# Optimization experiments

Hardware: AMD Instinct MI355X
Metric: run time of the kernel (lower is better)

## Reference

```python
import jax, jax.numpy as jnp
import numpy as np
import math

B, S, D = 4, 2048, 1024
H = 1
HD = D // H  # head_dim == hidden_dim since num_heads=1 (required by source's phase_encoder Linear)
HALF = HD // 2
SYNC_LOSS_WEIGHT = 0.01


def setup_inputs() -> dict:
    key = jax.random.key(0)
    ks = jax.random.split(key, 11)
    wstd = 0.02
    inp = {
        "x": jax.random.normal(ks[0], (B, S, D), dtype=jnp.float32),
        "Wq": jax.random.normal(ks[1], (D, D), dtype=jnp.float32) * wstd,
        "bq": jnp.zeros((D,), jnp.float32),
        "Wk": jax.random.normal(ks[2], (D, D), dtype=jnp.float32) * wstd,
        "bk": jnp.zeros((D,), jnp.float32),
        "Wv": jax.random.normal(ks[3], (D, D), dtype=jnp.float32) * wstd,
        "bv": jnp.zeros((D,), jnp.float32),
        "Wp": jax.random.normal(ks[4], (D, D), dtype=jnp.float32) * wstd,
        "bp": jnp.zeros((D,), jnp.float32),
        "Wo": jax.random.normal(ks[5], (D, D), dtype=jnp.float32) * wstd,
        "bo": jnp.zeros((D,), jnp.float32),
        "bifurcation_param": jnp.asarray(1.0, jnp.float32),
        "phase_coupling": jnp.asarray(0.5, jnp.float32),
    }
    return inp


def _phase(t, Wp, bp):
    # t: [B,H,S,HD] -> instantaneous phase via angle(complex(first_half, second_half))
    pf = t @ Wp.T + bp
    re, im = pf[..., :HALF], pf[..., HALF:]
    return jnp.arctan2(im, re)  # [B,H,S,HALF]


def reference(x, Wq, bq, Wk, bk, Wv, bv, Wp, bp, Wo, bo, bifurcation_param, phase_coupling):
    b, s, d = x.shape
    Q = (x @ Wq.T + bq).reshape(b, s, H, HD).transpose(0, 2, 1, 3)  # [B,H,S,HD]
    K = (x @ Wk.T + bk).reshape(b, s, H, HD).transpose(0, 2, 1, 3)
    V = (x @ Wv.T + bv).reshape(b, s, H, HD).transpose(0, 2, 1, 3)

    scores = jnp.einsum("bhqd,bhkd->bhqk", Q, K) / math.sqrt(HD)

    pQ = _phase(Q, Wp, bp)
    pK = _phase(K, Wp, bp)
    # mean_d cos(pQ - pK) == (cos(pQ)@cos(pK)^T + sin(pQ)@sin(pK)^T) / HALF
    sync = (jnp.einsum("bhqd,bhkd->bhqk", jnp.cos(pQ), jnp.cos(pK))
            + jnp.einsum("bhqd,bhkd->bhqk", jnp.sin(pQ), jnp.sin(pK))) / HALF

    t = jnp.tanh(scores)
    bif = bifurcation_param * t * (1.0 - t)

    chaotic = scores + phase_coupling * sync + bif
    attn = jax.nn.softmax(chaotic, axis=-1)

    av = jnp.einsum("bhqk,bhkd->bhqd", attn, V)
    av = av.transpose(0, 2, 1, 3).reshape(b, s, d)
    out = av @ Wo.T + bo

    # torch.var default: unbiased (ddof=1), over last dim of sync
    sync_loss = SYNC_LOSS_WEIGHT * jnp.var(sync, axis=-1, ddof=1).mean()
    return out, sync_loss
```

## Files before the change

### kernel.cpp

```cpp
#include <hip/hip_runtime.h>
#include <hip/hip_bf16.h>
#include <math.h>

#define S_LEN 2048
#define D_MODEL 1024
#define N_BATCH 4
#define N_HALF 512

typedef unsigned short u16;
typedef __attribute__((ext_vector_type(8))) short bf16x8;
typedef __attribute__((ext_vector_type(4))) float f32x4;

__device__ inline u16 f2bf(float v) {
  __hip_bfloat16 h = __float2bfloat16(v);
  return *reinterpret_cast<u16*>(&h);
}
__device__ inline float bf2f(u16 u) {
  __hip_bfloat16 h = *reinterpret_cast<__hip_bfloat16*>(&u);
  return __bfloat162float(h);
}
__device__ inline void gl2lds16(const void* g, void* l) {
  __builtin_amdgcn_global_load_lds(
      (const __attribute__((address_space(1))) unsigned int*)g,
      (__attribute__((address_space(3))) unsigned int*)l, 16, 0, 0);
}
__device__ inline float fast_tanh(float x) {
  float e = __expf(2.0f * x);
  return 1.0f - 2.0f / (e + 1.0f);
}

__global__ __launch_bounds__(256)
void cast_bf4(const float* __restrict__ src, u16* __restrict__ dst, long long n4) {
  long long i = (long long)blockIdx.x * 256 + threadIdx.x;
  if (i >= n4) return;
  float4 v = ((const float4*)src)[i];
  ushort4 o;
  o.x = f2bf(v.x); o.y = f2bf(v.y); o.z = f2bf(v.z); o.w = f2bf(v.w);
  ((ushort4*)dst)[i] = o;
}
__global__ __launch_bounds__(256)
void cast_split(const float* __restrict__ src, u16* __restrict__ hi,
                u16* __restrict__ lo, long long n) {
  long long i = (long long)blockIdx.x * 256 + threadIdx.x;
  if (i < n) {
    float v = src[i];
    u16 h = f2bf(v);
    hi[i] = h;
    lo[i] = f2bf(v - bf2f(h));
  }
}
__global__ __launch_bounds__(256)
void transpose_split(const float* __restrict__ src, u16* __restrict__ hi,
                     u16* __restrict__ lo) {
  __shared__ float t[32][33];
  const int bx = blockIdx.x * 32;
  const int by = blockIdx.y * 32;
  const int c = threadIdx.x & 31;
  const int r0 = (threadIdx.x >> 5) * 4;
#pragma unroll
  for (int r = 0; r < 4; r++)
    t[r0 + r][c] = src[(long long)(by + r0 + r) * D_MODEL + bx + c];
  __syncthreads();
#pragma unroll
  for (int r = 0; r < 4; r++) {
    float v = t[c][r0 + r];
    long long idx = (long long)(bx + r0 + r) * D_MODEL + by + c;
    u16 h = f2bf(v);
    hi[idx] = h;
    lo[idx] = f2bf(v - bf2f(h));
  }
}
__global__ __launch_bounds__(256)
void zero_stats(float* __restrict__ p, int n) {
  int i = blockIdx.x * 256 + threadIdx.x;
  if (i < n) p[i] = 0.f;
}
__global__ __launch_bounds__(256)
void w2_bias(const float* __restrict__ Wo, const float* __restrict__ bv,
             float* __restrict__ w2b) {
  const int d = blockIdx.x;
  const int tid = threadIdx.x;
  float acc = 0.f;
  for (int j = tid; j < D_MODEL; j += 256)
    acc += Wo[(long long)d * D_MODEL + j] * bv[j];
#pragma unroll
  for (int m = 1; m < 64; m <<= 1) acc += __shfl_xor(acc, m);
  __shared__ float red[4];
  if ((tid & 63) == 0) red[tid >> 6] = acc;
  __syncthreads();
  if (tid == 0) w2b[d] = red[0] + red[1] + red[2] + red[3];
}

__global__ __launch_bounds__(256, 2)
void qk_fused(const u16* __restrict__ X, const u16* __restrict__ Wq,
              const u16* __restrict__ Wk,
              const float* __restrict__ bq, const float* __restrict__ bk,
              u16* __restrict__ Qo, u16* __restrict__ Ko) {
  __shared__ u16 Xs[128 * 32];
  __shared__ u16 Qs[128 * 32];
  __shared__ u16 Ks[128 * 32];
  const int tid  = threadIdx.x;
  const int wave = tid >> 6;
  const int lane = tid & 63;
  const int quad = lane >> 4;
  const int tc   = lane & 15;
  const int bm = blockIdx.y * 128;
  const int bn = blockIdx.x * 128;
  const int wm = (wave & 1) * 64;
  const int wn = (wave >> 1) * 64;

  f32x4 acc1[4][4], acc2[4][4];
#pragma unroll
  for (int i = 0; i < 4; i++)
#pragma unroll
    for (int j = 0; j < 4; j++) {
      acc1[i][j] = (f32x4){0.f, 0.f, 0.f, 0.f};
      acc2[i][j] = (f32x4){0.f, 0.f, 0.f, 0.f};
    }

  const int srow = wave * 32 + (lane >> 2);
  const int scol = (lane & 3) * 8;
  const u16* gx = X  + (long long)(bm + srow) * D_MODEL + scol;
  const u16* gq = Wq + (long long)(bn + srow) * D_MODEL + scol;
  const u16* gk = Wk + (long long)(bn + srow) * D_MODEL + scol;
  const int wb = (wave * 32) * 32;
  const long long r16 = 16LL * D_MODEL;

  for (int k0 = 0; k0 < D_MODEL; k0 += 32) {
    gl2lds16(gx,       Xs + wb);
    gl2lds16(gx + r16, Xs + wb + 512);
    gl2lds16(gq,       Qs + wb);
    gl2lds16(gq + r16, Qs + wb + 512);
    gl2lds16(gk,       Ks + wb);
    gl2lds16(gk + r16, Ks + wb + 512);
    gx += 32; gq += 32; gk += 32;
    __syncthreads();
    bf16x8 af[4], bq4[4], bk4[4];
#pragma unroll
    for (int i = 0; i < 4; i++)
      af[i] = *(const bf16x8*)(Xs + (wm + i * 16 + tc) * 32 + quad * 8);
#pragma unroll
    for (int j = 0; j < 4; j++) {
      int o = (wn + j * 16 + tc) * 32 + quad * 8;
      bq4[j] = *(const bf16x8*)(Qs + o);
      bk4[j] = *(const bf16x8*)(Ks + o);
    }
#pragma unroll
    for (int i = 0; i < 4; i++)
#pragma unroll
      for (int j = 0; j < 4; j++) {
        acc1[i][j] = __builtin_amdgcn_mfma_f32_16x16x32_bf16(af[i], bq4[j], acc1[i][j], 0, 0, 0);
        acc2[i][j] = __builtin_amdgcn_mfma_f32_16x16x32_bf16(af[i], bk4[j], acc2[i][j], 0, 0, 0);
      }
    __syncthreads();
  }

#pragma unroll
  for (int i = 0; i < 4; i++) {
    const int row0 = bm + wm + i * 16 + quad * 4;
#pragma unroll
    for (int j = 0; j < 4; j++) {
      const int col = bn + wn + j * 16 + tc;
#pragma unroll
      for (int r = 0; r < 4; r++) {
        long long idx = (long long)(row0 + r) * D_MODEL + col;
        Qo[idx] = f2bf(acc1[i][j][r] + bq[col]);
        Ko[idx] = f2bf(acc2[i][j][r] + bk[col]);
      }
    }
  }
}

__global__ __launch_bounds__(256, 2)
void pf_fused(const u16* __restrict__ Qb, const u16* __restrict__ Wp,
              const float* __restrict__ bp,
              u16* __restrict__ pfQ, u16* __restrict__ pfK,
              long long TDo) {
  __shared__ u16 Qs[128 * 32];
  __shared__ u16 Ks[128 * 32];
  __shared__ u16 Ws[128 * 32];
  const int tid  = threadIdx.x;
  const int wave = tid >> 6;
  const int lane = tid & 63;
  const int quad = lane >> 4;
  const int tc   = lane & 15;
  const int bm = blockIdx.y * 128;
  const int bn = blockIdx.x * 128;
  const int wm = (wave & 1) * 64;
  const int wn = (wave >> 1) * 64;

  f32x4 acc1[4][4], acc2[4][4];
#pragma unroll
  for (int i = 0; i < 4; i++)
#pragma unroll
    for (int j = 0; j < 4; j++) {
      acc1[i][j] = (f32x4){0.f, 0.f, 0.f, 0.f};
      acc2[i][j] = (f32x4){0.f, 0.f, 0.f, 0.f};
    }

  const int srow = wave * 32 + (lane >> 2);
  const int scol = (lane & 3) * 8;
  const u16* gq = Qb + (long long)(bm + srow) * D_MODEL + scol;
  const u16* gk = gq + TDo;
  const u16* gw = Wp + (long long)(bn + srow) * D_MODEL + scol;
  const int wb = (wave * 32) * 32;
  const long long r16 = 16LL * D_MODEL;

  for (int k0 = 0; k0 < D_MODEL; k0 += 32) {
    gl2lds16(gq,       Qs + wb);
    gl2lds16(gq + r16, Qs + wb + 512);
    gl2lds16(gk,       Ks + wb);
    gl2lds16(gk + r16, Ks + wb + 512);
    gl2lds16(gw,       Ws + wb);
    gl2lds16(gw + r16, Ws + wb + 512);
    gq += 32; gk += 32; gw += 32;
    __syncthreads();
    bf16x8 aq[4], ak[4], bw[4];
#pragma unroll
    for (int i = 0; i < 4; i++) {
      int o = (wm + i * 16 + tc) * 32 + quad * 8;
      aq[i] = *(const bf16x8*)(Qs + o);
      ak[i] = *(const bf16x8*)(Ks + o);
    }
#pragma unroll
    for (int j = 0; j < 4; j++)
      bw[j] = *(const bf16x8*)(Ws + (wn + j * 16 + tc) * 32 + quad * 8);
#pragma unroll
    for (int i = 0; i < 4; i++)
#pragma unroll
      for (int j = 0; j < 4; j++) {
        acc1[i][j] = __builtin_amdgcn_mfma_f32_16x16x32_bf16(aq[i], bw[j], acc1[i][j], 0, 0, 0);
        acc2[i][j] = __builtin_amdgcn_mfma_f32_16x16x32_bf16(ak[i], bw[j], acc2[i][j], 0, 0, 0);
      }
    __syncthreads();
  }

#pragma unroll
  for (int i = 0; i < 4; i++) {
    const int row0 = bm + wm + i * 16 + quad * 4;
#pragma unroll
    for (int j = 0; j < 4; j++) {
      const int col = bn + wn + j * 16 + tc;
#pragma unroll
      for (int r = 0; r < 4; r++) {
        long long idx = (long long)(row0 + r) * D_MODEL + col;
        float b = bp[col];
        pfQ[idx] = f2bf(acc1[i][j][r] + b);
        pfK[idx] = f2bf(acc2[i][j][r] + b);
      }
    }
  }
}

__global__ __launch_bounds__(256)
void mfma_gemm_out3(const u16* __restrict__ Ah, const u16* __restrict__ Al,
                    const u16* __restrict__ Bh, const u16* __restrict__ Bl,
                    const float* __restrict__ bias, float* __restrict__ C,
                    int N, int K) {
  __shared__ u16 Ash[128 * 32];
  __shared__ u16 Asl[128 * 32];
  __shared__ u16 Bsh[128 * 32];
  __shared__ u16 Bsl[128 * 32];
  const int tid  = threadIdx.x;
  const int wave = tid >> 6;
  const int lane = tid & 63;
  const int quad = lane >> 4;
  const int tc   = lane & 15;
  const int bm = blockIdx.y * 128;
  const int bn = blockIdx.x * 128;
  const int wm = (wave & 1) * 64;
  const int wn = (wave >> 1) * 64;

  f32x4 acc[4][4];
#pragma unroll
  for (int i = 0; i < 4; i++)
#pragma unroll
    for (int j = 0; j < 4; j++) acc[i][j] = (f32x4){0.f, 0.f, 0.f, 0.f};

  const int srow = wave * 32 + (lane >> 2);
  const int scol = (lane & 3) * 8;
  long long aoff = (long long)(bm + srow) * K + scol;
  long long boff = (long long)(bn + srow) * K + scol;
  const u16 *gah = Ah + aoff, *gal = Al + aoff;
  const u16 *gbh = Bh + boff, *gbl = Bl + boff;
  const int wbase = (wave * 32) * 32;
  const long long r16K = 16LL * K;

  for (int k0 = 0; k0 < K; k0 += 32) {
    gl2lds16(gah,        Ash + wbase);
    gl2lds16(gah + r16K, Ash + wbase + 512);
    gl2lds16(gal,        Asl + wbase);
    gl2lds16(gal + r16K, Asl + wbase + 512);
    gl2lds16(gbh,        Bsh + wbase);
    gl2lds16(gbh + r16K, Bsh + wbase + 512);
    gl2lds16(gbl,        Bsl + wbase);
    gl2lds16(gbl + r16K, Bsl + wbase + 512);
    gah += 32; gal += 32; gbh += 32; gbl += 32;
    __syncthreads();
    bf16x8 ah[4], al[4], bh[4], bl[4];
#pragma unroll
    for (int i = 0; i < 4; i++) {
      int o = (wm + i * 16 + tc) * 32 + quad * 8;
      ah[i] = *(const bf16x8*)(Ash + o);
      al[i] = *(const bf16x8*)(Asl + o);
    }
#pragma unroll
    for (int j = 0; j < 4; j++) {
      int o = (wn + j * 16 + tc) * 32 + quad * 8;
      bh[j] = *(const bf16x8*)(Bsh + o);
      bl[j] = *(const bf16x8*)(Bsl + o);
    }
#pragma unroll
    for (int i = 0; i < 4; i++)
#pragma unroll
      for (int j = 0; j < 4; j++) {
        acc[i][j] = __builtin_amdgcn_mfma_f32_16x16x32_bf16(ah[i], bh[j], acc[i][j], 0, 0, 0);
        acc[i][j] = __builtin_amdgcn_mfma_f32_16x16x32_bf16(ah[i], bl[j], acc[i][j], 0, 0, 0);
        acc[i][j] = __builtin_amdgcn_mfma_f32_16x16x32_bf16(al[i], bh[j], acc[i][j], 0, 0, 0);
      }
    __syncthreads();
  }
#pragma unroll
  for (int i = 0; i < 4; i++) {
    const int row0 = bm + wm + i * 16 + quad * 4;
#pragma unroll
    for (int j = 0; j < 4; j++) {
      const int col = bn + wn + j * 16 + tc;
      float b = bias ? bias[col] : 0.f;
#pragma unroll
      for (int r = 0; r < 4; r++)
        C[(long long)(row0 + r) * N + col] = acc[i][j][r] + b;
    }
  }
}

__global__ __launch_bounds__(256)
void vwt_kernel(const u16* __restrict__ W2h, const u16* __restrict__ W2l,
                const u16* __restrict__ X, const float* __restrict__ w2b,
                u16* __restrict__ Ch, u16* __restrict__ Cl,
                long long sB, long long sC) {
  __shared__ u16 Ah[128 * 32];
  __shared__ u16 Al[128 * 32];
  __shared__ u16 Bs[128 * 32];
  const int tid  = threadIdx.x;
  const int wave = tid >> 6;
  const int lane = tid & 63;
  const int quad = lane >> 4;
  const int tc   = lane & 15;
  const int bm = blockIdx.y * 128;
  const int bn = blockIdx.x * 128;
  const long long z = blockIdx.z;
  const int wm = (wave & 1) * 64;
  const int wn = (wave >> 1) * 64;

  f32x4 acc[4][4];
#pragma unroll
  for (int i = 0; i < 4; i++)
#pragma unroll
    for (int j = 0; j < 4; j++) acc[i][j] = (f32x4){0.f, 0.f, 0.f, 0.f};

  const int srow = wave * 32 + (lane >> 2);
  const int scol = (lane & 3) * 8;
  const long long aoff = (long long)(bm + srow) * D_MODEL + scol;
  const u16* gah = W2h + aoff;
  const u16* gal = W2l + aoff;
  const u16* gb  = X + z * sB + (long long)(bn + srow) * D_MODEL + scol;
  const int wb = (wave * 32) * 32;
  const long long r16 = 16LL * D_MODEL;

  for (int k0 = 0; k0 < D_MODEL; k0 += 32) {
    gl2lds16(gah,       Ah + wb);
    gl2lds16(gah + r16, Ah + wb + 512);
    gl2lds16(gal,       Al + wb);
    gl2lds16(gal + r16, Al + wb + 512);
    gl2lds16(gb,        Bs + wb);
    gl2lds16(gb + r16,  Bs + wb + 512);
    gah += 32; gal += 32; gb += 32;
    __syncthreads();
    bf16x8 ah4[4], al4[4], bx[4];
#pragma unroll
    for (int i = 0; i < 4; i++) {
      int o = (wm + i * 16 + tc) * 32 + quad * 8;
      ah4[i] = *(const bf16x8*)(Ah + o);
      al4[i] = *(const bf16x8*)(Al + o);
    }
#pragma unroll
    for (int j = 0; j < 4; j++)
      bx[j] = *(const bf16x8*)(Bs + (wn + j * 16 + tc) * 32 + quad * 8);
#pragma unroll
    for (int i = 0; i < 4; i++)
#pragma unroll
      for (int j = 0; j < 4; j++) {
        acc[i][j] = __builtin_amdgcn_mfma_f32_16x16x32_bf16(ah4[i], bx[j], acc[i][j], 0, 0, 0);
        acc[i][j] = __builtin_amdgcn_mfma_f32_16x16x32_bf16(al4[i], bx[j], acc[i][j], 0, 0, 0);
      }
    __syncthreads();
  }

  u16* Chz = Ch + z * sC;
  u16* Clz = Cl + z * sC;
#pragma unroll
  for (int i = 0; i < 4; i++) {
    const int row0 = bm + wm + i * 16 + quad * 4;
#pragma unroll
    for (int j = 0; j < 4; j++) {
      const int col = bn + wn + j * 16 + tc;
#pragma unroll
      for (int r = 0; r < 4; r++) {
        float v = acc[i][j][r] + w2b[row0 + r];
        long long idx = (long long)(row0 + r) * S_LEN + col;
        u16 h = f2bf(v);
        Chz[idx] = h;
        Clz[idx] = f2bf(v - bf2f(h));
      }
    }
  }
}

__global__ __launch_bounds__(256)
void gemm_bsplit(const u16* __restrict__ A,
                 const u16* __restrict__ Bh, const u16* __restrict__ Bl,
                 const float* __restrict__ bias, float* __restrict__ C,
                 int N, int K, long long sA, long long sB, long long sC) {
  __shared__ u16 As[128 * 32];
  __shared__ u16 Bsh[128 * 32];
  __shared__ u16 Bsl[128 * 32];
  const int tid  = threadIdx.x;
  const int wave = tid >> 6;
  const int lane = tid & 63;
  const int quad = lane >> 4;
  const int tc   = lane & 15;
  const int bm = blockIdx.y * 128;
  const int bn = blockIdx.x * 128;
  const long long z = blockIdx.z;
  const int wm = (wave & 1) * 64;
  const int wn = (wave >> 1) * 64;

  f32x4 acc[4][4];
#pragma unroll
  for (int i = 0; i < 4; i++)
#pragma unroll
    for (int j = 0; j < 4; j++) acc[i][j] = (f32x4){0.f, 0.f, 0.f, 0.f};

  const int srow = wave * 32 + (lane >> 2);
  const int scol = (lane & 3) * 8;
  const long long boff = (long long)(bn + srow) * K + scol;
  const u16* ga  = A + z * sA + (long long)(bm + srow) * K + scol;
  const u16* gbh = Bh + z * sB + boff;
  const u16* gbl = Bl + z * sB + boff;
  const int wb = (wave * 32) * 32;
  const long long r16K = 16LL * K;

  for (int k0 = 0; k0 < K; k0 += 32) {
    gl2lds16(ga,         As + wb);
    gl2lds16(ga + r16K,  As + wb + 512);
    gl2lds16(gbh,        Bsh + wb);
    gl2lds16(gbh + r16K, Bsh + wb + 512);
    gl2lds16(gbl,        Bsl + wb);
    gl2lds16(gbl + r16K, Bsl + wb + 512);
    ga += 32; gbh += 32; gbl += 32;
    __syncthreads();
    bf16x8 af[4], bh[4], bl[4];
#pragma unroll
    for (int i = 0; i < 4; i++)
      af[i] = *(const bf16x8*)(As + (wm + i * 16 + tc) * 32 + quad * 8);
#pragma unroll
    for (int j = 0; j < 4; j++) {
      int o = (wn + j * 16 + tc) * 32 + quad * 8;
      bh[j] = *(const bf16x8*)(Bsh + o);
      bl[j] = *(const bf16x8*)(Bsl + o);
    }
#pragma unroll
    for (int i = 0; i < 4; i++)
#pragma unroll
      for (int j = 0; j < 4; j++) {
        acc[i][j] = __builtin_amdgcn_mfma_f32_16x16x32_bf16(af[i], bh[j], acc[i][j], 0, 0, 0);
        acc[i][j] = __builtin_amdgcn_mfma_f32_16x16x32_bf16(af[i], bl[j], acc[i][j], 0, 0, 0);
      }
    __syncthreads();
  }

  float* Cz = C + z * sC;
#pragma unroll
  for (int i = 0; i < 4; i++) {
    const int row0 = bm + wm + i * 16 + quad * 4;
#pragma unroll
    for (int j = 0; j < 4; j++) {
      const int col = bn + wn + j * 16 + tc;
#pragma unroll
      for (int r = 0; r < 4; r++)
        Cz[(long long)(row0 + r) * N + col] = acc[i][j][r] + bias[col];
    }
  }
}

__global__ __launch_bounds__(256, 2)
void chaotic_fused(const u16* __restrict__ Q, const u16* __restrict__ Kt,
                   const u16* __restrict__ Uq, const u16* __restrict__ Uk,
                   float* __restrict__ Cc,
                   float* __restrict__ ssum, float* __restrict__ ssq,
                   const float* __restrict__ bifp, const float* __restrict__ pcp) {
  __shared__ u16 Qs[128 * 32];
  __shared__ u16 Ks[128 * 32];
  __shared__ u16 Us[128 * 32];
  __shared__ u16 Ws[128 * 32];
  const int tid  = threadIdx.x;
  const int wave = tid >> 6;
  const int lane = tid & 63;
  const int quad = lane >> 4;
  const int tc   = lane & 15;
  const int bm = blockIdx.y * 128;
  const int bn = blockIdx.x * 128;
  const long long z = blockIdx.z;
  const long long sQ = (long long)S_LEN * D_MODEL;
  const int wm = (wave & 1) * 64;
  const int wn = (wave >> 1) * 64;

  f32x4 acc1[4][4], acc2[4][4];
#pragma unroll
  for (int i = 0; i < 4; i++)
#pragma unroll
    for (int j = 0; j < 4; j++) {
      acc1[i][j] = (f32x4){0.f, 0.f, 0.f, 0.f};
      acc2[i][j] = (f32x4){0.f, 0.f, 0.f, 0.f};
    }

  const int srow = wave * 32 + (lane >> 2);
  const int scol = (lane & 3) * 8;
  const long long aoff = (long long)(bm + srow) * D_MODEL + scol;
  const long long boff = (long long)(bn + srow) * D_MODEL + scol;
  const u16* gq = Q  + z * sQ + aoff;
  const u16* gk = Kt + z * sQ + boff;
  const u16* gu = Uq + z * sQ + aoff;
  const u16* gw = Uk + z * sQ + boff;
  const int wb = (wave * 32) * 32;
  const long long r16 = 16LL * D_MODEL;

  for (int k0 = 0; k0 < D_MODEL; k0 += 32) {
    gl2lds16(gq,       Qs + wb);
    gl2lds16(gq + r16, Qs + wb + 512);
    gl2lds16(gk,       Ks + wb);
    gl2lds16(gk + r16, Ks + wb + 512);
    gl2lds16(gu,       Us + wb);
    gl2lds16(gu + r16, Us + wb + 512);
    gl2lds16(gw,       Ws + wb);
    gl2lds16(gw + r16, Ws + wb + 512);
    gq += 32; gk += 32; gu += 32; gw += 32;
    __syncthreads();
    {
      bf16x8 af[4], bg[4];
#pragma unroll
      for (int i = 0; i < 4; i++)
        af[i] = *(const bf16x8*)(Qs + (wm + i * 16 + tc) * 32 + quad * 8);
#pragma unroll
      for (int j = 0; j < 4; j++)
        bg[j] = *(const bf16x8*)(Ks + (wn + j * 16 + tc) * 32 + quad * 8);
#pragma unroll
      for (int i = 0; i < 4; i++)
#pragma unroll
        for (int j = 0; j < 4; j++)
          acc1[i][j] = __builtin_amdgcn_mfma_f32_16x16x32_bf16(af[i], bg[j], acc1[i][j], 0, 0, 0);
    }
    {
      bf16x8 cf[4], dg[4];
#pragma unroll
      for (int i = 0; i < 4; i++)
        cf[i] = *(const bf16x8*)(Us + (wm + i * 16 + tc) * 32 + quad * 8);
#pragma unroll
      for (int j = 0; j < 4; j++)
        dg[j] = *(const bf16x8*)(Ws + (wn + j * 16 + tc) * 32 + quad * 8);
#pragma unroll
      for (int i = 0; i < 4; i++)
#pragma unroll
        for (int j = 0; j < 4; j++)
          acc2[i][j] = __builtin_amdgcn_mfma_f32_16x16x32_bf16(cf[i], dg[j], acc2[i][j], 0, 0, 0);
    }
    __syncthreads();
  }

  const float bif = *bifp;
  const float pc  = *pcp;
  float rsum[4][4], rsq[4][4];
#pragma unroll
  for (int i = 0; i < 4; i++)
#pragma unroll
    for (int r = 0; r < 4; r++) { rsum[i][r] = 0.f; rsq[i][r] = 0.f; }

  float* C = Cc + z * (long long)S_LEN * S_LEN;
#pragma unroll
  for (int i = 0; i < 4; i++) {
    const int row0 = bm + wm + i * 16 + quad * 4;
#pragma unroll
    for (int j = 0; j < 4; j++) {
      const int col = bn + wn + j * 16 + tc;
#pragma unroll
      for (int r = 0; r < 4; r++) {
        float sc = acc1[i][j][r] * 0.03125f;
        float sy = acc2[i][j][r] * (1.0f / 512.0f);
        float t  = fast_tanh(sc);
        C[(long long)(row0 + r) * S_LEN + col] = sc + pc * sy + bif * t * (1.0f - t);
        rsum[i][r] += sy;
        rsq[i][r]  += sy * sy;
      }
    }
  }
#pragma unroll
  for (int m = 1; m < 16; m <<= 1) {
#pragma unroll
    for (int i = 0; i < 4; i++)
#pragma unroll
      for (int r = 0; r < 4; r++) {
        rsum[i][r] += __shfl_xor(rsum[i][r], m);
        rsq[i][r]  += __shfl_xor(rsq[i][r], m);
      }
  }
  if (tc == 0) {
#pragma unroll
    for (int i = 0; i < 4; i++)
#pragma unroll
      for (int r = 0; r < 4; r++) {
        long long rr = z * S_LEN + bm + wm + i * 16 + quad * 4 + r;
        atomicAdd(&ssum[rr], rsum[i][r]);
        atomicAdd(&ssq[rr],  rsq[i][r]);
      }
  }
}

__global__ __launch_bounds__(256)
void phase_norm_bf(u16* __restrict__ U, long long n_rows) {
  long long idx = (long long)blockIdx.x * 256 + threadIdx.x;
  if (idx >= n_rows * N_HALF) return;
  long long row = idx >> 9;
  int j = (int)(idx & (N_HALF - 1));
  u16* p = U + row * D_MODEL;
  float re = bf2f(p[j]), im = bf2f(p[j + N_HALF]);
  float n2 = re * re + im * im;
  float cr = 1.f, sr = 0.f;
  if (n2 > 0.f) {
    float inv = 1.0f / sqrtf(n2);
    cr = re * inv; sr = im * inv;
  }
  p[j] = f2bf(cr); p[j + N_HALF] = f2bf(sr);
}

__global__ __launch_bounds__(256)
void softmax_bf(const float* __restrict__ Cc, u16* __restrict__ P) {
  const long long row = (long long)blockIdx.y * S_LEN + blockIdx.x;
  const float* p = Cc + row * S_LEN;
  u16* q = P + row * S_LEN;
  const int tid = threadIdx.x;
  float v[8];
  float m = -3.402823466e+38f;
#pragma unroll
  for (int i = 0; i < 8; i++) { v[i] = p[tid + i * 256]; m = fmaxf(m, v[i]); }
#pragma unroll
  for (int mask = 1; mask < 64; mask <<= 1) m = fmaxf(m, __shfl_xor(m, mask));
  __shared__ float red[8];
  if ((tid & 63) == 0) red[tid >> 6] = m;
  __syncthreads();
  m = fmaxf(fmaxf(red[0], red[1]), fmaxf(red[2], red[3]));
  float s = 0.f;
#pragma unroll
  for (int i = 0; i < 8; i++) { v[i] = __expf(v[i] - m); s += v[i]; }
#pragma unroll
  for (int mask = 1; mask < 64; mask <<= 1) s += __shfl_xor(s, mask);
  __syncthreads();
  if ((tid & 63) == 0) red[4 + (tid >> 6)] = s;
  __syncthreads();
  s = red[4] + red[5] + red[6] + red[7];
  float inv = 1.0f / s;
#pragma unroll
  for (int i = 0; i < 8; i++) q[tid + i * 256] = f2bf(v[i] * inv);
}

__global__ __launch_bounds__(1024)
void syncloss_kernel(const float* __restrict__ ssum, const float* __restrict__ ssq,
                     float* __restrict__ out) {
  const int tid = threadIdx.x;
  float acc = 0.f;
  for (int r = tid; r < N_BATCH * S_LEN; r += 1024) {
    float su = ssum[r], sq = ssq[r];
    acc += (sq - su * su * (1.0f / 2048.0f)) * (1.0f / 2047.0f);
  }
#pragma unroll
  for (int mask = 1; mask < 64; mask <<= 1) acc += __shfl_xor(acc, mask);
  __shared__ float red[16];
  if ((tid & 63) == 0) red[tid >> 6] = acc;
  __syncthreads();
  if (tid == 0) {
    float t = 0.f;
#pragma unroll
    for (int k = 0; k < 16; k++) t += red[k];
    out[0] = 0.01f * (t / (float)(N_BATCH * S_LEN));
  }
}

extern "C" void kernel_launch(void* const* d_in, const int* in_sizes, int n_in,
                              void* d_out, int out_size, void* d_ws, size_t ws_size,
                              hipStream_t stream) {
  const float* x    = (const float*)d_in[0];
  const float* Wq   = (const float*)d_in[1];
  const float* bq   = (const float*)d_in[2];
  const float* Wk   = (const float*)d_in[3];
  const float* bk   = (const float*)d_in[4];
  const float* Wv   = (const float*)d_in[5];
  const float* bv   = (const float*)d_in[6];
  const float* Wp   = (const float*)d_in[7];
  const float* bp   = (const float*)d_in[8];
  const float* Wo   = (const float*)d_in[9];
  const float* bo   = (const float*)d_in[10];
  const float* bifp = (const float*)d_in[11];
  const float* pcp  = (const float*)d_in[12];
  float* out = (float*)d_out;

  const long long NROW = (long long)N_BATCH * S_LEN;
  const long long TD   = NROW * D_MODEL;
  const long long WSZ  = (long long)D_MODEL * D_MODEL;

  u16* xbf   = (u16*)d_ws;
  u16* wqb   = xbf + TD;
  u16* wkb   = wqb + WSZ;
  u16* wpb   = wkb + WSZ;
  u16* woh   = wpb + WSZ;
  u16* wol   = woh + WSZ;
  u16* wvth  = wol + WSZ;
  u16* wvtl  = wvth + WSZ;
  u16* w2h   = wvtl + WSZ;
  u16* w2l   = w2h + WSZ;
  float* W2f = (float*)(w2l + WSZ);
  float* w2b = W2f + WSZ;
  u16* Qbf   = (u16*)(w2b + D_MODEL);
  u16* Kbf   = Qbf + TD;
  u16* pfQ   = Kbf + TD;
  u16* pfK   = pfQ + TD;
  float* Cc  = (float*)(pfK + TD);
  float* ssum = Cc + (long long)N_BATCH * S_LEN * S_LEN;
  float* ssq  = ssum + NROW;
  u16* attn = Qbf;
  u16* vwh  = pfQ;
  u16* vwl  = pfK;

  dim3 blk(256);
  const long long sQ = (long long)S_LEN * D_MODEL;
  const long long sS = (long long)S_LEN * S_LEN;

  cast_bf4<<<(int)(TD / 4 / 256), blk, 0, stream>>>(x, xbf, TD / 4);
  cast_bf4<<<(int)(WSZ / 4 / 256), blk, 0, stream>>>(Wq, wqb, WSZ / 4);
  cast_bf4<<<(int)(WSZ / 4 / 256), blk, 0, stream>>>(Wk, wkb, WSZ / 4);
  cast_bf4<<<(int)(WSZ / 4 / 256), blk, 0, stream>>>(Wp, wpb, WSZ / 4);
  cast_split<<<(int)(WSZ / 256), blk, 0, stream>>>(Wo, woh, wol, WSZ);
  transpose_split<<<dim3(32, 32), blk, 0, stream>>>(Wv, wvth, wvtl);
  mfma_gemm_out3<<<dim3(8, 8, 1), blk, 0, stream>>>(
      woh, wol, wvth, wvtl, nullptr, W2f, D_MODEL, D_MODEL);
  cast_split<<<(int)(WSZ / 256), blk, 0, stream>>>(W2f, w2h, w2l, WSZ);
  w2_bias<<<D_MODEL, blk, 0, stream>>>(Wo, bv, w2b);

  qk_fused<<<dim3(8, 64), blk, 0, stream>>>(xbf, wqb, wkb, bq, bk, Qbf, Kbf);
  pf_fused<<<dim3(8, 64), blk, 0, stream>>>(Qbf, wpb, bp, pfQ, pfK, TD);
  phase_norm_bf<<<(int)(2 * NROW * N_HALF / 256), blk, 0, stream>>>(pfQ, 2 * NROW);
  zero_stats<<<(int)((2 * NROW + 255) / 256), blk, 0, stream>>>(ssum, (int)(2 * NROW));

  chaotic_fused<<<dim3(16, 16, N_BATCH), blk, 0, stream>>>(
      Qbf, Kbf, pfQ, pfK, Cc, ssum, ssq, bifp, pcp);
  vwt_kernel<<<dim3(16, 8, N_BATCH), blk, 0, stream>>>(
      w2h, w2l, xbf, w2b, vwh, vwl, sQ, sQ);
  softmax_bf<<<dim3(S_LEN, N_BATCH), blk, 0, stream>>>(Cc, attn);
  gemm_bsplit<<<dim3(8, 16, N_BATCH), blk, 0, stream>>>(
      attn, vwh, vwl, bo, out,
      D_MODEL, S_LEN, sS, sQ, sQ);
  syncloss_kernel<<<1, 1024, 0, stream>>>(ssum, ssq, out + TD);
}
```

Before: 533.4 us.

## Deepen chaotic_fused K-tile to 64 with XOR-swizzled LDS, vectorize phase_norm

The fused score/sync GEMM kernel now stages 64-wide K slices instead of 32, which halves the number of loop iterations and barrier pairs. Its LDS layout uses an XOR swizzle on 16-byte chunks to avoid bank conflicts on the fragment reads. The phase normalisation kernel is rewritten to process 8 bf16 pairs per thread with 16-byte vector loads and stores. The cost is doubled LDS use (64KB per block), which may limit occupancy at launch_bounds(256,2), and more registers for the fragments.

```diff
diff --git a/kernel.cpp b/kernel.cpp
--- a/kernel.cpp
+++ b/kernel.cpp
@@ -500,10 +500,10 @@
                    float* __restrict__ Cc,
                    float* __restrict__ ssum, float* __restrict__ ssq,
                    const float* __restrict__ bifp, const float* __restrict__ pcp) {
-  __shared__ u16 Qs[128 * 32];
-  __shared__ u16 Ks[128 * 32];
-  __shared__ u16 Us[128 * 32];
-  __shared__ u16 Ws[128 * 32];
+  __shared__ u16 Qs[128 * 64];
+  __shared__ u16 Ks[128 * 64];
+  __shared__ u16 Us[128 * 64];
+  __shared__ u16 Ws[128 * 64];
   const int tid  = threadIdx.x;
   const int wave = tid >> 6;
   const int lane = tid & 63;
@@ -525,55 +525,69 @@
       acc2[i][j] = (f32x4){0.f, 0.f, 0.f, 0.f};
     }
 
-  const int srow = wave * 32 + (lane >> 2);
-  const int scol = (lane & 3) * 8;
-  const long long aoff = (long long)(bm + srow) * D_MODEL + scol;
-  const long long boff = (long long)(bn + srow) * D_MODEL + scol;
-  const u16* gq = Q  + z * sQ + aoff;
-  const u16* gk = Kt + z * sQ + boff;
-  const u16* gu = Uq + z * sQ + aoff;
-  const u16* gw = Uk + z * sQ + boff;
-  const int wb = (wave * 32) * 32;
-  const long long r16 = 16LL * D_MODEL;
-
-  for (int k0 = 0; k0 < D_MODEL; k0 += 32) {
-    gl2lds16(gq,       Qs + wb);
-    gl2lds16(gq + r16, Qs + wb + 512);
-    gl2lds16(gk,       Ks + wb);
-    gl2lds16(gk + r16, Ks + wb + 512);
-    gl2lds16(gu,       Us + wb);
-    gl2lds16(gu + r16, Us + wb + 512);
-    gl2lds16(gw,       Ws + wb);
-    gl2lds16(gw + r16, Ws + wb + 512);
-    gq += 32; gk += 32; gu += 32; gw += 32;
+  const int srow8  = lane >> 3;
+  const int scol   = ((lane & 7) ^ srow8) * 8;
+  const int srowb  = wave * 32;
+  const u16* gq = Q  + z * sQ + (long long)(bm + srowb + srow8) * D_MODEL + scol;
+  const u16* gk = Kt + z * sQ + (long long)(bn + srowb + srow8) * D_MODEL + scol;
+  const u16* gu = Uq + z * sQ + (long long)(bm + srowb + srow8) * D_MODEL + scol;
+  const u16* gw = Uk + z * sQ + (long long)(bn + srowb + srow8) * D_MODEL + scol;
+  const int wb = srowb * 64;
+  const long long r8 = 8LL * D_MODEL;
+
+  const int swzA = tc & 7;
+
+  for (int k0 = 0; k0 < D_MODEL; k0 += 64) {
+#pragma unroll
+    for (int c = 0; c < 4; c++) {
+      gl2lds16(gq + c * r8, Qs + wb + c * 512);
+      gl2lds16(gk + c * r8, Ks + wb + c * 512);
+      gl2lds16(gu + c * r8, Us + wb + c * 512);
+      gl2lds16(gw + c * r8, Ws + wb + c * 512);
+    }
+    gq += 64; gk += 64; gu += 64; gw += 64;
     __syncthreads();
     {
-      bf16x8 af[4], bg[4];
+      bf16x8 af[4][2], bg[4][2];
+#pragma unroll
+      for (int i = 0; i < 4; i++) {
+        const int ra = (wm + i * 16 + tc) * 64;
+        const int rb = (wn + i * 16 + tc) * 64;
+#pragma unroll
+        for (int ks = 0; ks < 2; ks++) {
+          const int co = ((ks * 4 + quad) ^ swzA) * 8;
+          af[i][ks] = *(const bf16x8*)(Qs + ra + co);
+          bg[i][ks] = *(const bf16x8*)(Ks + rb + co);
+        }
+      }
 #pragma unroll
       for (int i = 0; i < 4; i++)
-        af[i] = *(const bf16x8*)(Qs + (wm + i * 16 + tc) * 32 + quad * 8);
-#pragma unroll
-      for (int j = 0; j < 4; j++)
-        bg[j] = *(const bf16x8*)(Ks + (wn + j * 16 + tc) * 32 + quad * 8);
+#pragma unroll
+        for (int j = 0; j < 4; j++) {
+          acc1[i][j] = __builtin_amdgcn_mfma_f32_16x16x32_bf16(af[i][0], bg[j][0], acc1[i][j], 0, 0, 0);
+          acc1[i][j] = __builtin_amdgcn_mfma_f32_16x16x32_bf16(af[i][1], bg[j][1], acc1[i][j], 0, 0, 0);
+        }
+    }
+    {
+      bf16x8 cf[4][2], dg[4][2];
+#pragma unroll
+      for (int i = 0; i < 4; i++) {
+        const int ra = (wm + i * 16 + tc) * 64;
+        const int rb = (wn + i * 16 + tc) * 64;
+#pragma unroll
+        for (int ks = 0; ks < 2; ks++) {
+          const int co = ((ks * 4 + quad) ^ swzA) * 8;
+          cf[i][ks] = *(const bf16x8*)(Us + ra + co);
+          dg[i][ks] = *(const bf16x8*)(Ws + rb + co);
+        }
+      }
 #pragma unroll
       for (int i = 0; i < 4; i++)
 #pragma unroll
-        for (int j = 0; j < 4; j++)
-          acc1[i][j] = __builtin_amdgcn_mfma_f32_16x16x32_bf16(af[i], bg[j], acc1[i][j], 0, 0, 0);
-    }
-    {
-      bf16x8 cf[4], dg[4];
-#pragma unroll
-      for (int i = 0; i < 4; i++)
-        cf[i] = *(const bf16x8*)(Us + (wm + i * 16 + tc) * 32 + quad * 8);
-#pragma unroll
-      for (int j = 0; j < 4; j++)
-        dg[j] = *(const bf16x8*)(Ws + (wn + j * 16 + tc) * 32 + quad * 8);
-#pragma unroll
-      for (int i = 0; i < 4; i++)
-#pragma unroll
-        for (int j = 0; j < 4; j++)
-          acc2[i][j] = __builtin_amdgcn_mfma_f32_16x16x32_bf16(cf[i], dg[j], acc2[i][j], 0, 0, 0);
+        for (int j = 0; j < 4; j++) {
+          acc2[i][j] = __builtin_amdgcn_mfma_f32_16x16x32_bf16(cf[i][0], dg[j][0], acc2[i][j], 0, 0, 0);
+          acc2[i][j] = __builtin_amdgcn_mfma_f32_16x16x32_bf16(cf[i][1], dg[j][1], acc2[i][j], 0, 0, 0);
+        }
     }
     __syncthreads();
   }
@@ -629,18 +643,28 @@
 __global__ __launch_bounds__(256)
 void phase_norm_bf(u16* __restrict__ U, long long n_rows) {
   long long idx = (long long)blockIdx.x * 256 + threadIdx.x;
-  if (idx >= n_rows * N_HALF) return;
-  long long row = idx >> 9;
-  int j = (int)(idx & (N_HALF - 1));
-  u16* p = U + row * D_MODEL;
-  float re = bf2f(p[j]), im = bf2f(p[j + N_HALF]);
-  float n2 = re * re + im * im;
-  float cr = 1.f, sr = 0.f;
-  if (n2 > 0.f) {
-    float inv = 1.0f / sqrtf(n2);
-    cr = re * inv; sr = im * inv;
-  }
-  p[j] = f2bf(cr); p[j + N_HALF] = f2bf(sr);
+  if (idx >= n_rows * 64) return;
+  long long row = idx >> 6;
+  int j0 = (int)(idx & 63) * 8;
+  u16* p = U + row * D_MODEL + j0;
+  bf16x8 re8 = *(const bf16x8*)p;
+  bf16x8 im8 = *(const bf16x8*)(p + N_HALF);
+  bf16x8 ro, io;
+#pragma unroll
+  for (int i = 0; i < 8; i++) {
+    float re = bf2f((u16)re8[i]);
+    float im = bf2f((u16)im8[i]);
+    float n2 = re * re + im * im;
+    float cr = 1.f, sr = 0.f;
+    if (n2 > 0.f) {
+      float inv = 1.0f / sqrtf(n2);
+      cr = re * inv; sr = im * inv;
+    }
+    ro[i] = (short)f2bf(cr);
+    io[i] = (short)f2bf(sr);
+  }
+  *(bf16x8*)p = ro;
+  *(bf16x8*)(p + N_HALF) = io;
 }
 
 __global__ __launch_bounds__(256)
@@ -757,7 +781,7 @@
 
   qk_fused<<<dim3(8, 64), blk, 0, stream>>>(xbf, wqb, wkb, bq, bk, Qbf, Kbf);
   pf_fused<<<dim3(8, 64), blk, 0, stream>>>(Qbf, wpb, bp, pfQ, pfK, TD);
-  phase_norm_bf<<<(int)(2 * NROW * N_HALF / 256), blk, 0, stream>>>(pfQ, 2 * NROW);
+  phase_norm_bf<<<(int)(2 * NROW * 64 / 256), blk, 0, stream>>>(pfQ, 2 * NROW);
   zero_stats<<<(int)((2 * NROW + 255) / 256), blk, 0, stream>>>(ssum, (int)(2 * NROW));
 
   chaotic_fused<<<dim3(16, 16, N_BATCH), blk, 0, stream>>>(
```

After: 507.3 us. -4.9%, faster.
